# Kernel optimization log

Measured on AMD Instinct MI355X. Metric: run time of the kernel, lower is better.

The kernel has to match this reference:

```python
import jax, jax.numpy as jnp
import numpy as np

V, E, H, B, S, T = 32000, 512, 1024, 64, 128, 65

def setup_inputs() -> dict:
    key = jax.random.key(0)
    ks = jax.random.split(key, 10)
    f = lambda k, shape, s=1.0: jax.random.normal(k, shape, jnp.float32) * s
    return {
        "tgt_token_ids": jax.random.randint(ks[0], (T, B), 0, V),
        "enc_hidden": f(ks[1], (B, S, 2 * H)),
        "enc_mask": jnp.zeros((B, S), jnp.int32),  # 1 = masked (pad)
        "dec_init_hidden": f(ks[2], (B, H)),
        "dec_init_cell": f(ks[3], (B, H)),
        "embedding": f(ks[4], (V, E), 0.02),
        "W_ih": f(ks[5], (4 * H, E + H), 0.02),
        "W_hh": f(ks[6], (4 * H, H), 0.02),
        "b_ih": jnp.zeros((4 * H,), jnp.float32),
        "b_hh": jnp.zeros((4 * H,), jnp.float32),
        "W_att": f(ks[7], (H, 2 * H), 0.02),
        "W_comb": f(ks[8], (H, 3 * H), 0.02),
    }


def reference(tgt_token_ids, enc_hidden, enc_mask, dec_init_hidden, dec_init_cell,
              embedding, W_ih, W_hh, b_ih, b_hh, W_att, W_comb):
    mask = enc_mask.astype(bool)
    # enc_hiddens_proj = attention(enc_hidden): [B,S,2H] @ [H,2H].T -> [B,S,H]
    enc_proj = jnp.einsum('bsd,hd->bsh', enc_hidden, W_att)
    y = embedding[tgt_token_ids[:-1]]  # [T-1, B, E]
    # NOTE: faithful to the source, dec_init_state is fed to step() at EVERY
    # timestep (the updated LSTM state is discarded); only o_prev recurs.
    hh_term = dec_init_hidden @ W_hh.T + b_ih + b_hh  # [B, 4H], constant across steps
    c0 = dec_init_cell

    def step(o_prev, y_t):
        ybar = jnp.concatenate([y_t, o_prev], axis=1)        # [B, E+H]
        gates = ybar @ W_ih.T + hh_term                      # [B, 4H]
        i, f, g, o = jnp.split(gates, 4, axis=1)
        c = jax.nn.sigmoid(f) * c0 + jax.nn.sigmoid(i) * jnp.tanh(g)
        h = jax.nn.sigmoid(o) * jnp.tanh(c)                  # dec_hidden [B, H]
        e = jnp.einsum('bsh,bh->bs', enc_proj, h)            # scores [B, S]
        e = jnp.where(mask, -jnp.inf, e)
        alpha = jax.nn.softmax(e, axis=1)
        a = jnp.einsum('bs,bsd->bd', alpha, enc_hidden)      # context [B, 2H]
        U = jnp.concatenate([h, a], axis=1)                  # [B, 3H]
        O = jnp.tanh(U @ W_comb.T)                           # [B, H] (dropout = identity, eval)
        return O, O

    o0 = jnp.zeros_like(dec_init_hidden)
    _, outs = jax.lax.scan(step, o0, y)                      # [T-1, B, H]
    return outs
```

## Files before the change

kernel.cpp:

```cpp
#include <hip/hip_runtime.h>
#include <hip/hip_bf16.h>
#include <math.h>

#define BATCH 64
#define SRC   128
#define HID   1024
#define EMB   512
#define NT    64
#define G4    4096

__device__ __forceinline__ float sigmoidf_(float x){ return 1.0f/(1.0f+expf(-x)); }

template<int AMODE>
__launch_bounds__(256, 2)
__global__ void skinny_gemm(const float* __restrict__ A, int lda,
                            const int* __restrict__ toks, const float* __restrict__ emb,
                            const float* __restrict__ W, int ldw,
                            float* __restrict__ partial, int N, int Kchunk){
  const int nc = blockIdx.x;
  const int kc = blockIdx.y;
  const int kbase = kc * Kchunk;
  const int tid = threadIdx.x;
  __shared__ float As[16][64];
  __shared__ float Bs[16][128];
  const int wave = tid >> 6, lane = tid & 63;
  const int lm = lane & 7, ln = lane >> 3;
  const int nwave = nc*128 + wave*32;
  float acc[8][4] = {};
  const int arow = tid >> 2, akc = (tid & 3) * 4;
  for (int k0 = 0; k0 < Kchunk; k0 += 16){
    int kg = kbase + k0 + akc;
    float4 av;
    if (AMODE == 1){
      if (kg < EMB) av = *(const float4*)(emb + (size_t)toks[arow]*EMB + kg);
      else          av = *(const float4*)(A + (size_t)arow*lda + (kg - EMB));
    } else {
      av = *(const float4*)(A + (size_t)arow*lda + kg);
    }
    As[akc+0][arow]=av.x; As[akc+1][arow]=av.y; As[akc+2][arow]=av.z; As[akc+3][arow]=av.w;
    #pragma unroll
    for (int r = 0; r < 2; ++r){
      int idx = tid + r*256;
      int nrow = idx >> 2, bkc = (idx & 3) * 4;
      float4 wv = *(const float4*)(W + (size_t)(nc*128 + nrow)*ldw + kbase + k0 + bkc);
      Bs[bkc+0][nrow]=wv.x; Bs[bkc+1][nrow]=wv.y; Bs[bkc+2][nrow]=wv.z; Bs[bkc+3][nrow]=wv.w;
    }
    __syncthreads();
    #pragma unroll
    for (int k = 0; k < 16; ++k){
      float4 alo = *(const float4*)&As[k][lm*8];
      float4 ahi = *(const float4*)&As[k][lm*8+4];
      float4 b4  = *(const float4*)&Bs[k][wave*32 + ln*4];
      float am[8] = {alo.x,alo.y,alo.z,alo.w,ahi.x,ahi.y,ahi.z,ahi.w};
      float bn[4] = {b4.x,b4.y,b4.z,b4.w};
      #pragma unroll
      for (int i=0;i<8;++i)
        #pragma unroll
        for (int j=0;j<4;++j)
          acc[i][j] += am[i]*bn[j];
    }
    __syncthreads();
  }
  for (int i=0;i<8;++i){
    int m = lm*8+i;
    float4 v = make_float4(acc[i][0],acc[i][1],acc[i][2],acc[i][3]);
    *(float4*)(partial + ((size_t)(kc*64 + m))*N + nwave + ln*4) = v;
  }
}

__launch_bounds__(256, 2)
__global__ void big_gemm(const float* __restrict__ A, int lda,
                         const float* __restrict__ W, int ldw,
                         float* __restrict__ C, int N, int K){
  const int nc = blockIdx.x;
  const int m0 = blockIdx.y * 64;
  const int tid = threadIdx.x;
  __shared__ float As[16][64];
  __shared__ float Bs[16][128];
  const int wave = tid >> 6, lane = tid & 63;
  const int lm = lane & 7, ln = lane >> 3;
  const int nwave = nc*128 + wave*32;
  float acc[8][4] = {};
  const int arow = tid >> 2, akc = (tid & 3) * 4;
  for (int k0 = 0; k0 < K; k0 += 16){
    float4 av = *(const float4*)(A + (size_t)(m0+arow)*lda + k0 + akc);
    As[akc+0][arow]=av.x; As[akc+1][arow]=av.y; As[akc+2][arow]=av.z; As[akc+3][arow]=av.w;
    #pragma unroll
    for (int r = 0; r < 2; ++r){
      int idx = tid + r*256;
      int nrow = idx >> 2, bkc = (idx & 3) * 4;
      float4 wv = *(const float4*)(W + (size_t)(nc*128 + nrow)*ldw + k0 + bkc);
      Bs[bkc+0][nrow]=wv.x; Bs[bkc+1][nrow]=wv.y; Bs[bkc+2][nrow]=wv.z; Bs[bkc+3][nrow]=wv.w;
    }
    __syncthreads();
    #pragma unroll
    for (int k = 0; k < 16; ++k){
      float4 alo = *(const float4*)&As[k][lm*8];
      float4 ahi = *(const float4*)&As[k][lm*8+4];
      float4 b4  = *(const float4*)&Bs[k][wave*32 + ln*4];
      float am[8] = {alo.x,alo.y,alo.z,alo.w,ahi.x,ahi.y,ahi.z,ahi.w};
      float bn[4] = {b4.x,b4.y,b4.z,b4.w};
      #pragma unroll
      for (int i=0;i<8;++i)
        #pragma unroll
        for (int j=0;j<4;++j)
          acc[i][j] += am[i]*bn[j];
    }
    __syncthreads();
  }
  for (int i=0;i<8;++i){
    int m = m0 + lm*8+i;
    float4 v = make_float4(acc[i][0],acc[i][1],acc[i][2],acc[i][3]);
    *(float4*)(C + (size_t)m*N + nwave + ln*4) = v;
  }
}

__global__ void hh_reduce_kernel(const float* __restrict__ partial,
                                 const float* __restrict__ b_ih, const float* __restrict__ b_hh,
                                 float* __restrict__ hh_term){
  int g = blockIdx.x*512 + threadIdx.x;
  int n = g & 4095;
  int b = g >> 12;
  float s = b_ih[n] + b_hh[n];
  #pragma unroll
  for (int kc=0; kc<8; ++kc) s += partial[((size_t)(kc*64+b))*G4 + n];
  hh_term[g] = s;
}

__global__ void h_kernel(const float* __restrict__ partial, const float* __restrict__ hh_term,
                         const float* __restrict__ c0, float* __restrict__ h){
  int g = blockIdx.x*256 + threadIdx.x;
  int j = g & 1023;
  int b = g >> 10;
  float gate[4];
  #pragma unroll
  for (int q=0;q<4;++q){
    int n = q*HID + j;
    float s = hh_term[b*G4 + n];
    #pragma unroll
    for (int kc=0; kc<8; ++kc) s += partial[((size_t)(kc*64+b))*G4 + n];
    gate[q] = s;
  }
  float c = sigmoidf_(gate[1])*c0[g] + sigmoidf_(gate[0])*tanhf(gate[2]);
  h[g] = sigmoidf_(gate[3])*tanhf(c);
}

__launch_bounds__(512, 2)
__global__ void attn_kernel(const float* __restrict__ h, const float* __restrict__ enc_proj,
                            const float* __restrict__ encW, const int* __restrict__ enc_mask,
                            float* __restrict__ comb_a){
  const int b = blockIdx.x;
  const int tid = threadIdx.x;
  __shared__ float hs[HID];
  __shared__ float es[SRC];
  __shared__ float red[SRC];
  __shared__ float als[SRC];
  hs[tid] = h[b*HID + tid];
  hs[tid+512] = h[b*HID + 512 + tid];
  __syncthreads();
  const int wave = tid >> 6, lane = tid & 63;
  for (int s = wave*16; s < wave*16 + 16; ++s){
    const float* ep = enc_proj + ((size_t)b*SRC + s)*HID;
    float sum = 0.f;
    #pragma unroll
    for (int i=0;i<4;++i){
      float4 v  = *(const float4*)(ep + i*256 + lane*4);
      float4 hv = *(const float4*)&hs[i*256 + lane*4];
      sum += v.x*hv.x + v.y*hv.y + v.z*hv.z + v.w*hv.w;
    }
    #pragma unroll
    for (int off=32; off; off>>=1) sum += __shfl_down(sum, off);
    if (lane == 0) es[s] = sum;
  }
  __syncthreads();
  bool msk = false; float ev = 0.f;
  if (tid < SRC){
    ev = es[tid];
    msk = (enc_mask[b*SRC + tid] != 0);
    red[tid] = msk ? -1e30f : ev;
  }
  __syncthreads();
  for (int off=64; off>=1; off>>=1){ if (tid < off) red[tid] = fmaxf(red[tid], red[tid+off]); __syncthreads(); }
  float mval = red[0]; __syncthreads();
  float p = 0.f;
  if (tid < SRC && !msk) p = expf(ev - mval);
  if (tid < SRC) red[tid] = p;
  __syncthreads();
  for (int off=64; off>=1; off>>=1){ if (tid < off) red[tid] += red[tid+off]; __syncthreads(); }
  float ssum = red[0]; __syncthreads();
  if (tid < SRC) als[tid] = p / ssum;
  __syncthreads();
  const float* ew = encW + (size_t)b*SRC*HID;
  float acc0 = 0.f, acc1 = 0.f;
  #pragma unroll 4
  for (int s=0; s<SRC; ++s){
    float al = als[s];
    acc0 += al * ew[(size_t)s*HID + tid];
    acc1 += al * ew[(size_t)s*HID + 512 + tid];
  }
  comb_a[b*HID + tid] = acc0;
  comb_a[b*HID + 512 + tid] = acc1;
}

__global__ void final_O_kernel(const float* __restrict__ partial_c, const float* __restrict__ comb_a,
                               float* __restrict__ Obuf, float* __restrict__ out, int t){
  int g = blockIdx.x*512 + threadIdx.x;
  int n = g & 1023;
  int b = g >> 10;
  float s = comb_a[g];
  #pragma unroll
  for (int kc=0; kc<8; ++kc) s += partial_c[((size_t)(kc*64+b))*HID + n];
  float v = tanhf(s);
  Obuf[g] = v;
  out[(size_t)t*BATCH*HID + g] = v;
}

__global__ void zero_kernel(float* __restrict__ p, int n){
  int i = blockIdx.x*256 + threadIdx.x;
  if (i < n) p[i] = 0.f;
}

extern "C" void kernel_launch(void* const* d_in, const int* in_sizes, int n_in,
                              void* d_out, int out_size, void* d_ws, size_t ws_size,
                              hipStream_t stream) {
  const int*   tgt        = (const int*)d_in[0];
  const float* enc_hidden = (const float*)d_in[1];
  const int*   enc_mask   = (const int*)d_in[2];
  const float* dih        = (const float*)d_in[3];
  const float* dic        = (const float*)d_in[4];
  const float* emb        = (const float*)d_in[5];
  const float* W_ih       = (const float*)d_in[6];
  const float* W_hh       = (const float*)d_in[7];
  const float* b_ih       = (const float*)d_in[8];
  const float* b_hh       = (const float*)d_in[9];
  const float* W_att      = (const float*)d_in[10];
  const float* W_comb     = (const float*)d_in[11];
  float* out = (float*)d_out;

  float* ws        = (float*)d_ws;
  float* enc_proj  = ws;
  float* encW      = enc_proj + 8388608;
  float* partial_g = encW + 8388608;
  float* partial_c = partial_g + 2097152;
  float* hh_term   = partial_c + 524288;
  float* hbuf      = hh_term + 262144;
  float* comb_a    = hbuf + 65536;
  float* Obuf      = comb_a + 65536;

  big_gemm<<<dim3(8,128), 256, 0, stream>>>(enc_hidden, 2048, W_att, 2048, enc_proj, HID, 2048);
  big_gemm<<<dim3(8,128), 256, 0, stream>>>(enc_hidden, 2048, W_comb + HID, 3072, encW, HID, 2048);
  skinny_gemm<0><<<dim3(32,8), 256, 0, stream>>>(dih, HID, nullptr, nullptr, W_hh, HID, partial_g, G4, 128);
  hh_reduce_kernel<<<dim3(512), 512, 0, stream>>>(partial_g, b_ih, b_hh, hh_term);
  zero_kernel<<<dim3(256), 256, 0, stream>>>(Obuf, BATCH*HID);

  for (int t = 0; t < NT; ++t){
    skinny_gemm<1><<<dim3(32,8), 256, 0, stream>>>(Obuf, HID, tgt + t*BATCH, emb, W_ih, 1536, partial_g, G4, 192);
    h_kernel<<<dim3(256), 256, 0, stream>>>(partial_g, hh_term, dic, hbuf);
    skinny_gemm<0><<<dim3(8,8), 256, 0, stream>>>(hbuf, HID, nullptr, nullptr, W_comb, 3072, partial_c, HID, 128);
    attn_kernel<<<dim3(64), 512, 0, stream>>>(hbuf, enc_proj, encW, enc_mask, comb_a);
    final_O_kernel<<<dim3(128), 512, 0, stream>>>(partial_c, comb_a, Obuf, out, t);
  }
}
```

Before: 5.401 ms.

## Fuse LSTM cell with attention scores, fuse softmax/context/output, enlarge precompute GEMM tiles

Merges the gate/cell kernel with the attention score dot products, which are split into four hidden-dim chunks per batch row and reduced later. Softmax, the context weighting and the final tanh output are merged into one kernel split over four column chunks, so the comb_a buffer and one launch per step go away. The attention path is spread over 256 blocks instead of 64. The W_comb skinny GEMM now uses 16 K-splits and LDS tiles are padded to reduce bank conflicts. The precompute GEMMs use 128x128 tiles with an 8x8 register tile, which raises register pressure and redundantly recomputes softmax in each of the four chunk blocks.

```diff
diff --git a/kernel.cpp b/kernel.cpp
--- a/kernel.cpp
+++ b/kernel.cpp
@@ -21,8 +21,8 @@
   const int kc = blockIdx.y;
   const int kbase = kc * Kchunk;
   const int tid = threadIdx.x;
-  __shared__ float As[16][64];
-  __shared__ float Bs[16][128];
+  __shared__ float As[16][68];
+  __shared__ float Bs[16][132];
   const int wave = tid >> 6, lane = tid & 63;
   const int lm = lane & 7, ln = lane >> 3;
   const int nwave = nc*128 + wave*32;
@@ -69,49 +69,50 @@
 }
 
 __launch_bounds__(256, 2)
-__global__ void big_gemm(const float* __restrict__ A, int lda,
-                         const float* __restrict__ W, int ldw,
-                         float* __restrict__ C, int N, int K){
-  const int nc = blockIdx.x;
-  const int m0 = blockIdx.y * 64;
-  const int tid = threadIdx.x;
-  __shared__ float As[16][64];
-  __shared__ float Bs[16][128];
+__global__ void big_gemm128(const float* __restrict__ A, int lda,
+                            const float* __restrict__ W, int ldw,
+                            float* __restrict__ C, int N, int K){
+  const int n0 = blockIdx.x * 128;
+  const int m0 = blockIdx.y * 128;
+  const int tid = threadIdx.x;
+  __shared__ float As[16][132];
+  __shared__ float Bs[16][132];
   const int wave = tid >> 6, lane = tid & 63;
+  const int wm = wave >> 1, wn = wave & 1;
   const int lm = lane & 7, ln = lane >> 3;
-  const int nwave = nc*128 + wave*32;
-  float acc[8][4] = {};
-  const int arow = tid >> 2, akc = (tid & 3) * 4;
+  float acc[8][8] = {};
   for (int k0 = 0; k0 < K; k0 += 16){
-    float4 av = *(const float4*)(A + (size_t)(m0+arow)*lda + k0 + akc);
-    As[akc+0][arow]=av.x; As[akc+1][arow]=av.y; As[akc+2][arow]=av.z; As[akc+3][arow]=av.w;
     #pragma unroll
     for (int r = 0; r < 2; ++r){
       int idx = tid + r*256;
-      int nrow = idx >> 2, bkc = (idx & 3) * 4;
-      float4 wv = *(const float4*)(W + (size_t)(nc*128 + nrow)*ldw + k0 + bkc);
-      Bs[bkc+0][nrow]=wv.x; Bs[bkc+1][nrow]=wv.y; Bs[bkc+2][nrow]=wv.z; Bs[bkc+3][nrow]=wv.w;
+      int row = idx >> 2, kq = (idx & 3) * 4;
+      float4 av = *(const float4*)(A + (size_t)(m0+row)*lda + k0 + kq);
+      As[kq+0][row]=av.x; As[kq+1][row]=av.y; As[kq+2][row]=av.z; As[kq+3][row]=av.w;
+      float4 wv = *(const float4*)(W + (size_t)(n0+row)*ldw + k0 + kq);
+      Bs[kq+0][row]=wv.x; Bs[kq+1][row]=wv.y; Bs[kq+2][row]=wv.z; Bs[kq+3][row]=wv.w;
     }
     __syncthreads();
     #pragma unroll
     for (int k = 0; k < 16; ++k){
-      float4 alo = *(const float4*)&As[k][lm*8];
-      float4 ahi = *(const float4*)&As[k][lm*8+4];
-      float4 b4  = *(const float4*)&Bs[k][wave*32 + ln*4];
-      float am[8] = {alo.x,alo.y,alo.z,alo.w,ahi.x,ahi.y,ahi.z,ahi.w};
-      float bn[4] = {b4.x,b4.y,b4.z,b4.w};
+      float4 a0 = *(const float4*)&As[k][wm*64 + lm*8];
+      float4 a1 = *(const float4*)&As[k][wm*64 + lm*8 + 4];
+      float4 b0 = *(const float4*)&Bs[k][wn*64 + ln*8];
+      float4 b1 = *(const float4*)&Bs[k][wn*64 + ln*8 + 4];
+      float am[8] = {a0.x,a0.y,a0.z,a0.w,a1.x,a1.y,a1.z,a1.w};
+      float bn[8] = {b0.x,b0.y,b0.z,b0.w,b1.x,b1.y,b1.z,b1.w};
       #pragma unroll
       for (int i=0;i<8;++i)
         #pragma unroll
-        for (int j=0;j<4;++j)
+        for (int j=0;j<8;++j)
           acc[i][j] += am[i]*bn[j];
     }
     __syncthreads();
   }
   for (int i=0;i<8;++i){
-    int m = m0 + lm*8+i;
-    float4 v = make_float4(acc[i][0],acc[i][1],acc[i][2],acc[i][3]);
-    *(float4*)(C + (size_t)m*N + nwave + ln*4) = v;
+    int m = m0 + wm*64 + lm*8 + i;
+    float* cp = C + (size_t)m*N + n0 + wn*64 + ln*8;
+    *(float4*)cp     = make_float4(acc[i][0],acc[i][1],acc[i][2],acc[i][3]);
+    *(float4*)(cp+4) = make_float4(acc[i][4],acc[i][5],acc[i][6],acc[i][7]);
   }
 }
 
@@ -127,92 +128,72 @@
   hh_term[g] = s;
 }
 
-__global__ void h_kernel(const float* __restrict__ partial, const float* __restrict__ hh_term,
-                         const float* __restrict__ c0, float* __restrict__ h){
-  int g = blockIdx.x*256 + threadIdx.x;
-  int j = g & 1023;
-  int b = g >> 10;
+__global__ void h_e_kernel(const float* __restrict__ partial_g, const float* __restrict__ hh_term,
+                           const float* __restrict__ c0, const float* __restrict__ enc_proj,
+                           float* __restrict__ hbuf, float* __restrict__ e_part){
+  const int b = blockIdx.x, ch = blockIdx.y;
+  const int tid = threadIdx.x;
+  __shared__ float hs[256];
+  const int j = ch*256 + tid;
   float gate[4];
   #pragma unroll
   for (int q=0;q<4;++q){
     int n = q*HID + j;
     float s = hh_term[b*G4 + n];
     #pragma unroll
-    for (int kc=0; kc<8; ++kc) s += partial[((size_t)(kc*64+b))*G4 + n];
-    gate[q] = s;
-  }
-  float c = sigmoidf_(gate[1])*c0[g] + sigmoidf_(gate[0])*tanhf(gate[2]);
-  h[g] = sigmoidf_(gate[3])*tanhf(c);
-}
-
-__launch_bounds__(512, 2)
-__global__ void attn_kernel(const float* __restrict__ h, const float* __restrict__ enc_proj,
-                            const float* __restrict__ encW, const int* __restrict__ enc_mask,
-                            float* __restrict__ comb_a){
-  const int b = blockIdx.x;
-  const int tid = threadIdx.x;
-  __shared__ float hs[HID];
-  __shared__ float es[SRC];
+    for (int kc=0;kc<8;++kc) s += partial_g[((size_t)(kc*64+b))*G4 + n];
+    gate[q]=s;
+  }
+  float c = sigmoidf_(gate[1])*c0[b*HID+j] + sigmoidf_(gate[0])*tanhf(gate[2]);
+  float h = sigmoidf_(gate[3])*tanhf(c);
+  hs[tid] = h;
+  hbuf[b*HID + j] = h;
+  __syncthreads();
+  const int wave = tid>>6, lane = tid&63;
+  float4 hv = *(const float4*)&hs[lane*4];
+  for (int s = wave; s < SRC; s += 4){
+    const float* ep = enc_proj + ((size_t)b*SRC + s)*HID + ch*256;
+    float4 v = *(const float4*)(ep + lane*4);
+    float sum = v.x*hv.x + v.y*hv.y + v.z*hv.z + v.w*hv.w;
+    #pragma unroll
+    for (int off=32; off; off>>=1) sum += __shfl_down(sum, off);
+    if (lane==0) e_part[(b*4 + ch)*SRC + s] = sum;
+  }
+}
+
+__global__ void soft_comb_kernel(const float* __restrict__ e_part, const int* __restrict__ enc_mask,
+                                 const float* __restrict__ encW, const float* __restrict__ partial_c,
+                                 float* __restrict__ Obuf, float* __restrict__ out, int t){
+  const int b = blockIdx.x, ch = blockIdx.y;
+  const int tid = threadIdx.x;
+  __shared__ float als[SRC];
   __shared__ float red[SRC];
-  __shared__ float als[SRC];
-  hs[tid] = h[b*HID + tid];
-  hs[tid+512] = h[b*HID + 512 + tid];
-  __syncthreads();
-  const int wave = tid >> 6, lane = tid & 63;
-  for (int s = wave*16; s < wave*16 + 16; ++s){
-    const float* ep = enc_proj + ((size_t)b*SRC + s)*HID;
-    float sum = 0.f;
-    #pragma unroll
-    for (int i=0;i<4;++i){
-      float4 v  = *(const float4*)(ep + i*256 + lane*4);
-      float4 hv = *(const float4*)&hs[i*256 + lane*4];
-      sum += v.x*hv.x + v.y*hv.y + v.z*hv.z + v.w*hv.w;
-    }
-    #pragma unroll
-    for (int off=32; off; off>>=1) sum += __shfl_down(sum, off);
-    if (lane == 0) es[s] = sum;
-  }
-  __syncthreads();
-  bool msk = false; float ev = 0.f;
+  float ev = 0.f; bool msk = false;
   if (tid < SRC){
-    ev = es[tid];
-    msk = (enc_mask[b*SRC + tid] != 0);
+    ev = e_part[(b*4+0)*SRC+tid] + e_part[(b*4+1)*SRC+tid]
+       + e_part[(b*4+2)*SRC+tid] + e_part[(b*4+3)*SRC+tid];
+    msk = (enc_mask[b*SRC+tid] != 0);
     red[tid] = msk ? -1e30f : ev;
   }
   __syncthreads();
-  for (int off=64; off>=1; off>>=1){ if (tid < off) red[tid] = fmaxf(red[tid], red[tid+off]); __syncthreads(); }
+  for (int off=64; off>=1; off>>=1){ if (tid<off) red[tid]=fmaxf(red[tid],red[tid+off]); __syncthreads(); }
   float mval = red[0]; __syncthreads();
-  float p = 0.f;
-  if (tid < SRC && !msk) p = expf(ev - mval);
-  if (tid < SRC) red[tid] = p;
-  __syncthreads();
-  for (int off=64; off>=1; off>>=1){ if (tid < off) red[tid] += red[tid+off]; __syncthreads(); }
-  float ssum = red[0]; __syncthreads();
-  if (tid < SRC) als[tid] = p / ssum;
-  __syncthreads();
-  const float* ew = encW + (size_t)b*SRC*HID;
-  float acc0 = 0.f, acc1 = 0.f;
-  #pragma unroll 4
-  for (int s=0; s<SRC; ++s){
-    float al = als[s];
-    acc0 += al * ew[(size_t)s*HID + tid];
-    acc1 += al * ew[(size_t)s*HID + 512 + tid];
-  }
-  comb_a[b*HID + tid] = acc0;
-  comb_a[b*HID + 512 + tid] = acc1;
-}
-
-__global__ void final_O_kernel(const float* __restrict__ partial_c, const float* __restrict__ comb_a,
-                               float* __restrict__ Obuf, float* __restrict__ out, int t){
-  int g = blockIdx.x*512 + threadIdx.x;
-  int n = g & 1023;
-  int b = g >> 10;
-  float s = comb_a[g];
+  float p = (tid<SRC && !msk) ? expf(ev-mval) : 0.f;
+  if (tid<SRC) red[tid]=p;
+  __syncthreads();
+  for (int off=64; off>=1; off>>=1){ if (tid<off) red[tid]+=red[tid+off]; __syncthreads(); }
+  if (tid<SRC) als[tid] = p/red[0];
+  __syncthreads();
+  const int j = ch*256 + tid;
+  const float* ew = encW + (size_t)b*SRC*HID + j;
+  float acc = 0.f;
+  #pragma unroll 8
+  for (int s=0;s<SRC;++s) acc += als[s]*ew[(size_t)s*HID];
   #pragma unroll
-  for (int kc=0; kc<8; ++kc) s += partial_c[((size_t)(kc*64+b))*HID + n];
-  float v = tanhf(s);
-  Obuf[g] = v;
-  out[(size_t)t*BATCH*HID + g] = v;
+  for (int kc=0;kc<16;++kc) acc += partial_c[((size_t)(kc*64+b))*HID + j];
+  float v = tanhf(acc);
+  Obuf[b*HID+j] = v;
+  out[(size_t)t*BATCH*HID + b*HID + j] = v;
 }
 
 __global__ void zero_kernel(float* __restrict__ p, int n){
@@ -242,22 +223,21 @@
   float* encW      = enc_proj + 8388608;
   float* partial_g = encW + 8388608;
   float* partial_c = partial_g + 2097152;
-  float* hh_term   = partial_c + 524288;
+  float* hh_term   = partial_c + 1048576;
   float* hbuf      = hh_term + 262144;
-  float* comb_a    = hbuf + 65536;
-  float* Obuf      = comb_a + 65536;
-
-  big_gemm<<<dim3(8,128), 256, 0, stream>>>(enc_hidden, 2048, W_att, 2048, enc_proj, HID, 2048);
-  big_gemm<<<dim3(8,128), 256, 0, stream>>>(enc_hidden, 2048, W_comb + HID, 3072, encW, HID, 2048);
+  float* e_part    = hbuf + 65536;
+  float* Obuf      = e_part + 32768;
+
+  big_gemm128<<<dim3(8,64), 256, 0, stream>>>(enc_hidden, 2048, W_att, 2048, enc_proj, HID, 2048);
+  big_gemm128<<<dim3(8,64), 256, 0, stream>>>(enc_hidden, 2048, W_comb + HID, 3072, encW, HID, 2048);
   skinny_gemm<0><<<dim3(32,8), 256, 0, stream>>>(dih, HID, nullptr, nullptr, W_hh, HID, partial_g, G4, 128);
   hh_reduce_kernel<<<dim3(512), 512, 0, stream>>>(partial_g, b_ih, b_hh, hh_term);
   zero_kernel<<<dim3(256), 256, 0, stream>>>(Obuf, BATCH*HID);
 
   for (int t = 0; t < NT; ++t){
     skinny_gemm<1><<<dim3(32,8), 256, 0, stream>>>(Obuf, HID, tgt + t*BATCH, emb, W_ih, 1536, partial_g, G4, 192);
-    h_kernel<<<dim3(256), 256, 0, stream>>>(partial_g, hh_term, dic, hbuf);
-    skinny_gemm<0><<<dim3(8,8), 256, 0, stream>>>(hbuf, HID, nullptr, nullptr, W_comb, 3072, partial_c, HID, 128);
-    attn_kernel<<<dim3(64), 512, 0, stream>>>(hbuf, enc_proj, encW, enc_mask, comb_a);
-    final_O_kernel<<<dim3(128), 512, 0, stream>>>(partial_c, comb_a, Obuf, out, t);
-  }
-}
+    h_e_kernel<<<dim3(64,4), 256, 0, stream>>>(partial_g, hh_term, dic, enc_proj, hbuf, e_part);
+    skinny_gemm<0><<<dim3(8,16), 256, 0, stream>>>(hbuf, HID, nullptr, nullptr, W_comb, 3072, partial_c, HID, 64);
+    soft_comb_kernel<<<dim3(64,4), 256, 0, stream>>>(e_part, enc_mask, encW, partial_c, Obuf, out, t);
+  }
+}
```

Result: faster. 5.166 ms (-4.3%).
